# Performance work log

Measured on AMD Instinct MI355X. Metric: run time of the kernel, lower is better.

Reference implementation:

```python
import jax, jax.numpy as jnp
import numpy as np
from jax import lax

BITW = 1
BITA = 3


def _ste_round(x, n):
    # round with straight-through gradient (Round -> Identity override)
    return x + lax.stop_gradient(jnp.round(x * n) / n - x)


def _quantize_active(x, bitA):
    # cabs: clip |x| to [0, 1], then k-bit uniform quantization with STE round
    x = jnp.minimum(1.0, jnp.abs(x))
    if bitA == 32:
        return x
    n = float(2 ** bitA - 1)
    return _ste_round(x, n)


def _quantize_weight(w, bitW):
    if bitW == 32:
        return w
    if bitW == 1:
        # sign with STE (Sign -> Identity): grad w.r.t. w is 1
        E = lax.stop_gradient(jnp.mean(jnp.abs(w)))
        y = w / E
        return (y + lax.stop_gradient(jnp.sign(y) - y)) * E
    n = float(2 ** bitW - 1)
    w = jnp.clip(w * 0.5 + 0.5, 0.0, 1.0)
    return 2.0 * _ste_round(w, n) - 1.0


def setup_inputs() -> dict:
    key = jax.random.key(0)
    kx, kw, kb = jax.random.split(key, 3)
    x = jax.random.normal(kx, (32, 56, 56, 256), dtype=jnp.float32)
    W = jax.random.normal(kw, (3, 3, 256, 256), dtype=jnp.float32) * 0.02  # HWIO
    b = jax.random.normal(kb, (256,), dtype=jnp.float32) * 0.01
    return {"x": x, "W": W, "b": b}


def reference(x, W, b):
    xq = _quantize_active(x, BITA)          # [N,H,W,C] quantized activations
    wq = _quantize_weight(W, BITW)          # [kh,kw,Cin,Cout] binarized weights
    out = lax.conv_general_dilated(
        xq, wq,
        window_strides=(1, 1),
        padding="SAME",
        dimension_numbers=("NHWC", "HWIO", "NHWC"),
    )
    return out + b  # act = identity
```

## Files before the change

kernel.cpp:

```cpp
#include <hip/hip_runtime.h>

typedef __attribute__((ext_vector_type(4))) int int4v;
typedef __attribute__((ext_vector_type(16))) int int16v;

#define NPIX 100352
#define KTAP 2304
#define LDK 144

__global__ __launch_bounds__(256) void quant_w_kernel(const float* __restrict__ Wm,
                                                      signed char* __restrict__ Bt,
                                                      float* __restrict__ Esum) {
  __shared__ signed char sT[64][80];
  __shared__ float red[4];
  const int k0 = blockIdx.x * 64;
  const int c0 = blockIdx.y * 64;
  const int t = threadIdx.x;
  const int cc = t & 63;
  const int r0 = (t >> 6) * 16;
  float s = 0.f;
#pragma unroll
  for (int i = 0; i < 16; ++i) {
    const int k = r0 + i;
    float w = Wm[(long)(k0 + k) * 256 + c0 + cc];
    s += fabsf(w);
    sT[cc][k] = (signed char)((w > 0.f) ? 1 : ((w < 0.f) ? -1 : 0));
  }
#pragma unroll
  for (int o = 32; o > 0; o >>= 1) s += __shfl_down(s, o, 64);
  if ((t & 63) == 0) red[t >> 6] = s;
  __syncthreads();
  if (t == 0) atomicAdd(Esum, red[0] + red[1] + red[2] + red[3]);
  const int co = t >> 2;
  const int kc = (t & 3) * 16;
  int4v v = *(const int4v*)&sT[co][kc];
  *(int4v*)(Bt + (long)(c0 + co) * KTAP + k0 + kc) = v;
}

__global__ __launch_bounds__(256) void quant_x_kernel(const float* __restrict__ x,
                                                      signed char* __restrict__ xq) {
  int t = blockIdx.x * 256 + threadIdx.x;
  float4 v = ((const float4*)x)[t];
  unsigned int q = 0;
  q |= (unsigned int)(int)rintf(fminf(1.f, fabsf(v.x)) * 7.f);
  q |= ((unsigned int)(int)rintf(fminf(1.f, fabsf(v.y)) * 7.f)) << 8;
  q |= ((unsigned int)(int)rintf(fminf(1.f, fabsf(v.z)) * 7.f)) << 16;
  q |= ((unsigned int)(int)rintf(fminf(1.f, fabsf(v.w)) * 7.f)) << 24;
  ((unsigned int*)xq)[t] = q;
}

__global__ __launch_bounds__(256, 2) void conv_kernel(const signed char* __restrict__ xq,
                                                      const signed char* __restrict__ Bt,
                                                      const float* __restrict__ bias,
                                                      const float* __restrict__ Esum,
                                                      float* __restrict__ out) {
  __shared__ signed char As[128 * LDK];
  __shared__ signed char Bs[256 * LDK];

  const int t = threadIdx.x;
  const int lane = t & 63;
  const int wid = t >> 6;
  const int m0 = blockIdx.x * 128;
  const int wm = (wid & 1) * 64;
  const int wn = (wid >> 1) * 128;

  const int rbase = t >> 3;
  const int colb = (t & 7) * 16;

  int abase[4];
  unsigned avalid[4];
#pragma unroll
  for (int i = 0; i < 4; ++i) {
    const int p = m0 + rbase + 32 * i;
    const int rem = p % 3136;
    const int h = rem / 56, w = rem % 56;
    abase[i] = p * 256 + colb;
    unsigned mask = 0;
#pragma unroll
    for (int tap = 0; tap < 9; ++tap) {
      const int dh = tap / 3 - 1, dw = tap % 3 - 1;
      if ((unsigned)(h + dh) < 56u && (unsigned)(w + dw) < 56u) mask |= 1u << tap;
    }
    avalid[i] = mask;
  }
  int bofs[8];
#pragma unroll
  for (int i = 0; i < 8; ++i) bofs[i] = (rbase + 32 * i) * KTAP + colb;

  int16v acc[2][4];
#pragma unroll
  for (int a = 0; a < 2; ++a)
#pragma unroll
    for (int b = 0; b < 4; ++b)
#pragma unroll
      for (int r = 0; r < 16; ++r) acc[a][b][r] = 0;

  int4v ra[4], rb[8];

  auto prefetch = [&](int s) {
    const int tap = s >> 1, hf = s & 1;
    const int dh = tap / 3 - 1, dw = tap % 3 - 1;
    const int shift = (dh * 56 + dw) * 256 + hf * 128;
    const int kofs = tap * 256 + hf * 128;
#pragma unroll
    for (int i = 0; i < 4; ++i) {
      int4v a = {0, 0, 0, 0};
      if (avalid[i] & (1u << tap)) a = *(const int4v*)(xq + (long)(abase[i] + shift));
      ra[i] = a;
    }
#pragma unroll
    for (int i = 0; i < 8; ++i) rb[i] = *(const int4v*)(Bt + (long)(bofs[i] + kofs));
  };

  prefetch(0);
  const int lrow = lane & 31;
  const int khalf = (lane >> 5) * 16;

  for (int s = 0; s < 18; ++s) {
    if (s) __syncthreads();
#pragma unroll
    for (int i = 0; i < 4; ++i)
      *(int4v*)(As + (rbase + 32 * i) * LDK + colb) = ra[i];
#pragma unroll
    for (int i = 0; i < 8; ++i)
      *(int4v*)(Bs + (rbase + 32 * i) * LDK + colb) = rb[i];
    __syncthreads();
    if (s + 1 < 18) prefetch(s + 1);
#pragma unroll
    for (int ks = 0; ks < 4; ++ks) {
      const int ko = ks * 32 + khalf;
      int4v a0 = *(const int4v*)(As + (wm + lrow) * LDK + ko);
      int4v a1 = *(const int4v*)(As + (wm + 32 + lrow) * LDK + ko);
      int4v b0 = *(const int4v*)(Bs + (wn + lrow) * LDK + ko);
      int4v b1 = *(const int4v*)(Bs + (wn + 32 + lrow) * LDK + ko);
      int4v b2 = *(const int4v*)(Bs + (wn + 64 + lrow) * LDK + ko);
      int4v b3 = *(const int4v*)(Bs + (wn + 96 + lrow) * LDK + ko);
      acc[0][0] = __builtin_amdgcn_mfma_i32_32x32x32_i8(a0, b0, acc[0][0], 0, 0, 0);
      acc[0][1] = __builtin_amdgcn_mfma_i32_32x32x32_i8(a0, b1, acc[0][1], 0, 0, 0);
      acc[0][2] = __builtin_amdgcn_mfma_i32_32x32x32_i8(a0, b2, acc[0][2], 0, 0, 0);
      acc[0][3] = __builtin_amdgcn_mfma_i32_32x32x32_i8(a0, b3, acc[0][3], 0, 0, 0);
      acc[1][0] = __builtin_amdgcn_mfma_i32_32x32x32_i8(a1, b0, acc[1][0], 0, 0, 0);
      acc[1][1] = __builtin_amdgcn_mfma_i32_32x32x32_i8(a1, b1, acc[1][1], 0, 0, 0);
      acc[1][2] = __builtin_amdgcn_mfma_i32_32x32x32_i8(a1, b2, acc[1][2], 0, 0, 0);
      acc[1][3] = __builtin_amdgcn_mfma_i32_32x32x32_i8(a1, b3, acc[1][3], 0, 0, 0);
    }
  }

  const float scale = Esum[0] * (1.0f / (589824.0f * 7.0f));
#pragma unroll
  for (int mt = 0; mt < 2; ++mt)
#pragma unroll
    for (int nt = 0; nt < 4; ++nt) {
      const int col = wn + nt * 32 + lrow;
      const float bv = bias[col];
#pragma unroll
      for (int r = 0; r < 16; ++r) {
        const int row = (r & 3) + 8 * (r >> 2) + 4 * (lane >> 5);
        const int m = m0 + wm + mt * 32 + row;
        out[(long)m * 256 + col] = (float)acc[mt][nt][r] * scale + bv;
      }
    }
}

extern "C" void kernel_launch(void* const* d_in, const int* in_sizes, int n_in,
                              void* d_out, int out_size, void* d_ws, size_t ws_size,
                              hipStream_t stream) {
  const float* x    = (const float*)d_in[0];
  const float* Wm   = (const float*)d_in[1];
  const float* bias = (const float*)d_in[2];
  float* out = (float*)d_out;

  float* Esum = (float*)d_ws;
  signed char* Bt = (signed char*)d_ws + 256;
  signed char* xq = (signed char*)d_ws + 256 + 589824;

  hipMemsetAsync(d_ws, 0, 4, stream);
  quant_w_kernel<<<dim3(36, 4), 256, 0, stream>>>(Wm, Bt, Esum);
  quant_x_kernel<<<25088, 256, 0, stream>>>(x, xq);
  conv_kernel<<<784, 256, 0, stream>>>(xq, Bt, bias, Esum, out);
}
```

Baseline: 251.8 us.

## Pad quantized activations, load A operands directly to registers, double-buffer B in LDS

```diff
diff --git a/kernel.cpp b/kernel.cpp
--- a/kernel.cpp
+++ b/kernel.cpp
@@ -4,8 +4,10 @@
 typedef __attribute__((ext_vector_type(16))) int int16v;
 
 #define NPIX 100352
+#define PPIX 107648
 #define KTAP 2304
 #define LDK 144
+#define BSZ (256 * LDK)
 
 __global__ __launch_bounds__(256) void quant_w_kernel(const float* __restrict__ Wm,
                                                       signed char* __restrict__ Bt,
@@ -38,14 +40,28 @@
 
 __global__ __launch_bounds__(256) void quant_x_kernel(const float* __restrict__ x,
                                                       signed char* __restrict__ xq) {
-  int t = blockIdx.x * 256 + threadIdx.x;
-  float4 v = ((const float4*)x)[t];
-  unsigned int q = 0;
-  q |= (unsigned int)(int)rintf(fminf(1.f, fabsf(v.x)) * 7.f);
-  q |= ((unsigned int)(int)rintf(fminf(1.f, fabsf(v.y)) * 7.f)) << 8;
-  q |= ((unsigned int)(int)rintf(fminf(1.f, fabsf(v.z)) * 7.f)) << 16;
-  q |= ((unsigned int)(int)rintf(fminf(1.f, fabsf(v.w)) * 7.f)) << 24;
-  ((unsigned int*)xq)[t] = q;
+  const int tid = blockIdx.x * 256 + threadIdx.x;
+  const int ci = tid & 63;
+  const int pix = tid >> 6;
+  const int q1 = pix / 58;
+  const int wp = pix - q1 * 58;
+  const int n = q1 / 58;
+  const int hp = q1 - n * 58;
+  unsigned int qv = 0;
+  if ((unsigned)(hp - 1) < 56u && (unsigned)(wp - 1) < 56u) {
+    const int src = n * 3136 + (hp - 1) * 56 + (wp - 1);
+    float4 v = ((const float4*)x)[src * 64 + ci];
+    qv  = (unsigned int)(int)rintf(fminf(1.f, fabsf(v.x)) * 7.f);
+    qv |= ((unsigned int)(int)rintf(fminf(1.f, fabsf(v.y)) * 7.f)) << 8;
+    qv |= ((unsigned int)(int)rintf(fminf(1.f, fabsf(v.z)) * 7.f)) << 16;
+    qv |= ((unsigned int)(int)rintf(fminf(1.f, fabsf(v.w)) * 7.f)) << 24;
+  }
+  ((unsigned int*)xq)[tid] = qv;
+}
+
+__device__ __forceinline__ int tap_shift(int u) {
+  const int tp = u >> 1;
+  return ((tp / 3 - 1) * 58 + (tp % 3) - 1) * 256 + (u & 1) * 128;
 }
 
 __global__ __launch_bounds__(256, 2) void conv_kernel(const signed char* __restrict__ xq,
@@ -53,95 +69,104 @@
                                                       const float* __restrict__ bias,
                                                       const float* __restrict__ Esum,
                                                       float* __restrict__ out) {
-  __shared__ signed char As[128 * LDK];
-  __shared__ signed char Bs[256 * LDK];
+  __shared__ signed char Bs[2 * BSZ];
 
   const int t = threadIdx.x;
   const int lane = t & 63;
   const int wid = t >> 6;
-  const int m0 = blockIdx.x * 128;
+  const int bid = blockIdx.x;
+  const int tile = (bid & 7) * 98 + (bid >> 3);
+  const int m0 = tile * 128;
   const int wm = (wid & 1) * 64;
   const int wn = (wid >> 1) * 128;
-
-  const int rbase = t >> 3;
-  const int colb = (t & 7) * 16;
-
-  int abase[4];
-  unsigned avalid[4];
-#pragma unroll
-  for (int i = 0; i < 4; ++i) {
-    const int p = m0 + rbase + 32 * i;
-    const int rem = p % 3136;
-    const int h = rem / 56, w = rem % 56;
-    abase[i] = p * 256 + colb;
-    unsigned mask = 0;
-#pragma unroll
-    for (int tap = 0; tap < 9; ++tap) {
-      const int dh = tap / 3 - 1, dw = tap % 3 - 1;
-      if ((unsigned)(h + dh) < 56u && (unsigned)(w + dw) < 56u) mask |= 1u << tap;
-    }
-    avalid[i] = mask;
-  }
-  int bofs[8];
-#pragma unroll
-  for (int i = 0; i < 8; ++i) bofs[i] = (rbase + 32 * i) * KTAP + colb;
-
-  int16v acc[2][4];
-#pragma unroll
-  for (int a = 0; a < 2; ++a)
-#pragma unroll
-    for (int b = 0; b < 4; ++b)
-#pragma unroll
-      for (int r = 0; r < 16; ++r) acc[a][b][r] = 0;
-
-  int4v ra[4], rb[8];
-
-  auto prefetch = [&](int s) {
-    const int tap = s >> 1, hf = s & 1;
-    const int dh = tap / 3 - 1, dw = tap % 3 - 1;
-    const int shift = (dh * 56 + dw) * 256 + hf * 128;
-    const int kofs = tap * 256 + hf * 128;
-#pragma unroll
-    for (int i = 0; i < 4; ++i) {
-      int4v a = {0, 0, 0, 0};
-      if (avalid[i] & (1u << tap)) a = *(const int4v*)(xq + (long)(abase[i] + shift));
-      ra[i] = a;
-    }
-#pragma unroll
-    for (int i = 0; i < 8; ++i) rb[i] = *(const int4v*)(Bt + (long)(bofs[i] + kofs));
-  };
-
-  prefetch(0);
   const int lrow = lane & 31;
   const int khalf = (lane >> 5) * 16;
 
+  int pb0, pb1;
+  {
+    const int p0 = m0 + wm + lrow;
+    const int n0 = p0 / 3136, r0 = p0 - n0 * 3136;
+    const int h0 = r0 / 56, w0 = r0 - h0 * 56;
+    pb0 = ((n0 * 58 + h0 + 1) * 58 + (w0 + 1)) * 256 + khalf;
+    const int p1 = p0 + 32;
+    const int n1 = p1 / 3136, r1 = p1 - n1 * 3136;
+    const int h1 = r1 / 56, w1 = r1 - h1 * 56;
+    pb1 = ((n1 * 58 + h1 + 1) * 58 + (w1 + 1)) * 256 + khalf;
+  }
+
+  const int brow = t >> 3;
+  const int bcol = (t & 7) * 16;
+  const int gb = brow * KTAP + bcol;
+  const int lb = brow * LDK + bcol;
+
+  int16v acc[2][4];
+#pragma unroll
+  for (int a = 0; a < 2; ++a)
+#pragma unroll
+    for (int b = 0; b < 4; ++b)
+#pragma unroll
+      for (int r = 0; r < 16; ++r) acc[a][b][r] = 0;
+
+  int4v raA0 = *(const int4v*)(xq + pb0 + tap_shift(0));
+  int4v raA1 = *(const int4v*)(xq + pb1 + tap_shift(0));
+  int4v rb[8];
+#pragma unroll
+  for (int i = 0; i < 8; ++i) rb[i] = *(const int4v*)(Bt + gb + i * (32 * KTAP));
+#pragma unroll
+  for (int i = 0; i < 8; ++i) *(int4v*)(Bs + lb + i * (32 * LDK)) = rb[i];
+#pragma unroll
+  for (int i = 0; i < 8; ++i) rb[i] = *(const int4v*)(Bt + gb + 128 + i * (32 * KTAP));
+  asm volatile("s_waitcnt lgkmcnt(0)" ::: "memory");
+  __builtin_amdgcn_s_barrier();
+  __builtin_amdgcn_sched_barrier(0);
+
   for (int s = 0; s < 18; ++s) {
-    if (s) __syncthreads();
-#pragma unroll
-    for (int i = 0; i < 4; ++i)
-      *(int4v*)(As + (rbase + 32 * i) * LDK + colb) = ra[i];
-#pragma unroll
-    for (int i = 0; i < 8; ++i)
-      *(int4v*)(Bs + (rbase + 32 * i) * LDK + colb) = rb[i];
-    __syncthreads();
-    if (s + 1 < 18) prefetch(s + 1);
+    const int ash = tap_shift(s);
+    const int ashN = tap_shift(s < 17 ? s + 1 : 17);
+    signed char* Bcur = Bs + (s & 1) * BSZ;
+    signed char* Bnxt = Bs + ((~s) & 1) * BSZ;
+    const signed char* a0p = xq + pb0 + ash;
+    const signed char* a1p = xq + pb1 + ash;
+    const signed char* n0p = xq + pb0 + ashN;
+    const signed char* n1p = xq + pb1 + ashN;
+
+    if (s + 1 < 18) {
+#pragma unroll
+      for (int i = 0; i < 8; ++i) *(int4v*)(Bnxt + lb + i * (32 * LDK)) = rb[i];
+    }
+    if (s + 2 < 18) {
+      const int ko2 = (s + 2) * 128;
+#pragma unroll
+      for (int i = 0; i < 8; ++i) rb[i] = *(const int4v*)(Bt + gb + ko2 + i * (32 * KTAP));
+    }
+
 #pragma unroll
     for (int ks = 0; ks < 4; ++ks) {
+      int4v nx0 = *(const int4v*)((ks < 3) ? (a0p + (ks + 1) * 32) : n0p);
+      int4v nx1 = *(const int4v*)((ks < 3) ? (a1p + (ks + 1) * 32) : n1p);
       const int ko = ks * 32 + khalf;
-      int4v a0 = *(const int4v*)(As + (wm + lrow) * LDK + ko);
-      int4v a1 = *(const int4v*)(As + (wm + 32 + lrow) * LDK + ko);
-      int4v b0 = *(const int4v*)(Bs + (wn + lrow) * LDK + ko);
-      int4v b1 = *(const int4v*)(Bs + (wn + 32 + lrow) * LDK + ko);
-      int4v b2 = *(const int4v*)(Bs + (wn + 64 + lrow) * LDK + ko);
-      int4v b3 = *(const int4v*)(Bs + (wn + 96 + lrow) * LDK + ko);
-      acc[0][0] = __builtin_amdgcn_mfma_i32_32x32x32_i8(a0, b0, acc[0][0], 0, 0, 0);
-      acc[0][1] = __builtin_amdgcn_mfma_i32_32x32x32_i8(a0, b1, acc[0][1], 0, 0, 0);
-      acc[0][2] = __builtin_amdgcn_mfma_i32_32x32x32_i8(a0, b2, acc[0][2], 0, 0, 0);
-      acc[0][3] = __builtin_amdgcn_mfma_i32_32x32x32_i8(a0, b3, acc[0][3], 0, 0, 0);
-      acc[1][0] = __builtin_amdgcn_mfma_i32_32x32x32_i8(a1, b0, acc[1][0], 0, 0, 0);
-      acc[1][1] = __builtin_amdgcn_mfma_i32_32x32x32_i8(a1, b1, acc[1][1], 0, 0, 0);
-      acc[1][2] = __builtin_amdgcn_mfma_i32_32x32x32_i8(a1, b2, acc[1][2], 0, 0, 0);
-      acc[1][3] = __builtin_amdgcn_mfma_i32_32x32x32_i8(a1, b3, acc[1][3], 0, 0, 0);
+      int4v b0 = *(const int4v*)(Bcur + (wn + lrow) * LDK + ko);
+      int4v b1 = *(const int4v*)(Bcur + (wn + 32 + lrow) * LDK + ko);
+      int4v b2 = *(const int4v*)(Bcur + (wn + 64 + lrow) * LDK + ko);
+      int4v b3 = *(const int4v*)(Bcur + (wn + 96 + lrow) * LDK + ko);
+      __builtin_amdgcn_s_setprio(1);
+      acc[0][0] = __builtin_amdgcn_mfma_i32_32x32x32_i8(raA0, b0, acc[0][0], 0, 0, 0);
+      acc[0][1] = __builtin_amdgcn_mfma_i32_32x32x32_i8(raA0, b1, acc[0][1], 0, 0, 0);
+      acc[0][2] = __builtin_amdgcn_mfma_i32_32x32x32_i8(raA0, b2, acc[0][2], 0, 0, 0);
+      acc[0][3] = __builtin_amdgcn_mfma_i32_32x32x32_i8(raA0, b3, acc[0][3], 0, 0, 0);
+      acc[1][0] = __builtin_amdgcn_mfma_i32_32x32x32_i8(raA1, b0, acc[1][0], 0, 0, 0);
+      acc[1][1] = __builtin_amdgcn_mfma_i32_32x32x32_i8(raA1, b1, acc[1][1], 0, 0, 0);
+      acc[1][2] = __builtin_amdgcn_mfma_i32_32x32x32_i8(raA1, b2, acc[1][2], 0, 0, 0);
+      acc[1][3] = __builtin_amdgcn_mfma_i32_32x32x32_i8(raA1, b3, acc[1][3], 0, 0, 0);
+      __builtin_amdgcn_s_setprio(0);
+      raA0 = nx0; raA1 = nx1;
+    }
+
+    if (s < 17) {
+      asm volatile("s_waitcnt lgkmcnt(0)" ::: "memory");
+      __builtin_amdgcn_sched_barrier(0);
+      __builtin_amdgcn_s_barrier();
+      __builtin_amdgcn_sched_barrier(0);
     }
   }
 
@@ -175,6 +200,6 @@
 
   hipMemsetAsync(d_ws, 0, 4, stream);
   quant_w_kernel<<<dim3(36, 4), 256, 0, stream>>>(Wm, Bt, Esum);
-  quant_x_kernel<<<25088, 256, 0, stream>>>(x, xq);
+  quant_x_kernel<<<26912, 256, 0, stream>>>(x, xq);
   conv_kernel<<<784, 256, 0, stream>>>(xq, Bt, bias, Esum, out);
 }
```

Measured after the change: 271.7 us. 1.08x slower.
